# Kernel optimization log

Measured on AMD Instinct MI355X. Metric: run time of the kernel, lower is better.

## Reference

```python
import jax, jax.numpy as jnp
import numpy as np
import math

B, S, E = 2, 2048, 1024
H = 16                      # n_state_heads
STATE_SIZE = 16384
O = math.isqrt(STATE_SIZE // H)   # state_head_order = 32
C = E // (O * H)            # embedding_state_head_order_chunk_size = 2
N_BLOCKS = 12
EPS = 1e-5


def layernorm(x, g):
    mu = jnp.mean(x, axis=-1, keepdims=True)
    var = jnp.mean(jnp.square(x - mu), axis=-1, keepdims=True)
    return (x - mu) * jax.lax.rsqrt(var + EPS) * g


def setup_inputs() -> dict:
    key = jax.random.key(0)
    ks = jax.random.split(key, 8)
    return {
        "activations": jax.random.normal(ks[0], (B, S, E), dtype=jnp.float32),
        # note: torch init zeros W_up; we use small random weights so the scan is non-trivial
        "W_up": jax.random.normal(ks[1], (O, C), dtype=jnp.float32) * 0.02,
        "W_down": jax.random.normal(ks[2], (C, O), dtype=jnp.float32) * (0.02 * math.sqrt(STATE_SIZE)),
        "W_mru": jax.random.normal(ks[3], (E, E), dtype=jnp.float32) * (0.02 / math.sqrt(N_BLOCKS)),
        "g_ln1": jnp.ones((E,), dtype=jnp.float32),
        "g_ln2": jnp.ones((E,), dtype=jnp.float32),
        "W_mlp1": jax.random.normal(ks[4], (4 * E, E), dtype=jnp.float32) * 0.02,
        "W_mlp2": jax.random.normal(ks[5], (E, 4 * E), dtype=jnp.float32) * (0.02 / math.sqrt(N_BLOCKS)),
    }


def reference(activations, W_up, W_down, W_mru, g_ln1, g_ln2, W_mlp1, W_mlp2):
    x = activations                                   # [B,S,E]
    h = layernorm(x, g_ln1)
    hh = h.reshape(B, S, H, O, C)                     # unflatten(-1, (H, O, C))
    # state_matrices_up (Linear C->O, no bias) + eye  -> per-token transition matrices
    M = jnp.einsum('bshoc,qc->bshoq', hh, W_up) + jnp.eye(O, dtype=h.dtype)  # [B,S,H,O,O]
    Mt = jnp.swapaxes(M, 1, 2)                        # [B,H,S,O,O]
    # cumulative non-commutative matrix products along the sequence (log-depth scan)
    P = jax.lax.associative_scan(jnp.matmul, Mt, axis=2)  # P[t] = M_0 @ ... @ M_t
    states = jnp.swapaxes(P, 1, 2)                    # [B,S,H,O,O]
    # state_matrices_down (Linear O->C, no bias), then flatten(-3,-1)
    down = jnp.einsum('bshoq,cq->bshoc', states, W_down).reshape(B, S, E)
    mru_out = down @ W_mru.T
    x = x + mru_out
    y = layernorm(x, g_ln2)
    m = jax.nn.gelu(y @ W_mlp1.T, approximate=False) @ W_mlp2.T
    x = x + m
    new_state = states[-1]                            # faithful to torch states[-1] (last batch element): [S,H,O,O]
    return (x, new_state)
```

## Files before the change

kernel.cpp:

```cpp
#include <hip/hip_runtime.h>
#include <hip/hip_bf16.h>
#include <math.h>

#define Bb 2
#define Ss 2048
#define Ee 1024
#define Hh 16
#define Oo 32
#define Cc 2
#define EPSf 1e-5f
#define NSEG 64
#define SEGL 32
#define NGRP 8
#define GRPL 8

typedef __hip_bfloat16 bf16;
typedef __attribute__((ext_vector_type(8))) short short8;
typedef __attribute__((ext_vector_type(4))) float f32x4;

template <typename OT>
__global__ __launch_bounds__(256) void ln_kernel(const float* __restrict__ x,
                                                 const float* __restrict__ g,
                                                 OT* __restrict__ out) {
    __shared__ float red[8];
    int row = blockIdx.x;
    const float4* xr = (const float4*)(x + (size_t)row * Ee);
    float4 v = xr[threadIdx.x];
    float s = v.x + v.y + v.z + v.w;
#pragma unroll
    for (int off = 32; off > 0; off >>= 1) s += __shfl_xor(s, off);
    int wave = threadIdx.x >> 6, lane = threadIdx.x & 63;
    if (!lane) red[wave] = s;
    __syncthreads();
    float mu = (red[0] + red[1] + red[2] + red[3]) * (1.0f / Ee);
    float dx = v.x - mu, dy = v.y - mu, dz = v.z - mu, dw = v.w - mu;
    float sq = dx * dx + dy * dy + dz * dz + dw * dw;
#pragma unroll
    for (int off = 32; off > 0; off >>= 1) sq += __shfl_xor(sq, off);
    if (!lane) red[wave + 4] = sq;
    __syncthreads();
    float var = (red[4] + red[5] + red[6] + red[7]) * (1.0f / Ee);
    float rs = rsqrtf(var + EPSf);
    float4 gv = ((const float4*)g)[threadIdx.x];
    float o0 = dx * rs * gv.x, o1 = dy * rs * gv.y, o2 = dz * rs * gv.z, o3 = dw * rs * gv.w;
    if constexpr (sizeof(OT) == 4) {
        ((float4*)((float*)out + (size_t)row * Ee))[threadIdx.x] = make_float4(o0, o1, o2, o3);
    } else {
        __align__(8) bf16 t[4] = {__float2bfloat16(o0), __float2bfloat16(o1),
                                  __float2bfloat16(o2), __float2bfloat16(o3)};
        ((ushort4*)((unsigned short*)out + (size_t)row * Ee))[threadIdx.x] = *(const ushort4*)t;
    }
}

__device__ __forceinline__ void cvt4(const float* in, bf16* out, int i) {
    float4 v = ((const float4*)in)[i];
    __align__(8) bf16 t[4] = {__float2bfloat16(v.x), __float2bfloat16(v.y),
                              __float2bfloat16(v.z), __float2bfloat16(v.w)};
    ((ushort4*)out)[i] = *(const ushort4*)t;
}

__global__ __launch_bounds__(256) void prep_kernel(const float* __restrict__ act,
                                                   const float* __restrict__ g,
                                                   float* __restrict__ hs,
                                                   const float* __restrict__ wa, bf16* __restrict__ oa,
                                                   const float* __restrict__ wb, bf16* __restrict__ ob,
                                                   const float* __restrict__ wc, bf16* __restrict__ oc) {
    int bid = blockIdx.x;
    if (bid < Bb * Ss) {
        __shared__ float red[8];
        int row = bid;
        const float4* xr = (const float4*)(act + (size_t)row * Ee);
        float4 v = xr[threadIdx.x];
        float s = v.x + v.y + v.z + v.w;
#pragma unroll
        for (int off = 32; off > 0; off >>= 1) s += __shfl_xor(s, off);
        int wave = threadIdx.x >> 6, lane = threadIdx.x & 63;
        if (!lane) red[wave] = s;
        __syncthreads();
        float mu = (red[0] + red[1] + red[2] + red[3]) * (1.0f / Ee);
        float dx = v.x - mu, dy = v.y - mu, dz = v.z - mu, dw = v.w - mu;
        float sq = dx * dx + dy * dy + dz * dz + dw * dw;
#pragma unroll
        for (int off = 32; off > 0; off >>= 1) sq += __shfl_xor(sq, off);
        if (!lane) red[wave + 4] = sq;
        __syncthreads();
        float var = (red[4] + red[5] + red[6] + red[7]) * (1.0f / Ee);
        float rs = rsqrtf(var + EPSf);
        float4 gv = ((const float4*)g)[threadIdx.x];
        float o0 = dx * rs * gv.x, o1 = dy * rs * gv.y, o2 = dz * rs * gv.z, o3 = dw * rs * gv.w;
        int b = row >> 11, t = row & 2047;
        int e0 = threadIdx.x * 4;
        int head = e0 >> 6;
        float* dst = hs + (((size_t)(b * Hh + head) * Ss) + t) * 64 + (e0 & 63);
        *(float4*)dst = make_float4(o0, o1, o2, o3);
    } else {
        int i = (bid - Bb * Ss) * 256 + threadIdx.x;
        const int nA = (1024 * 1024) / 4;
        const int nB = (4 * 1024 * 1024) / 4;
        if (i < nA) cvt4(wa, oa, i);
        else if (i < nA + nB) cvt4(wb, ob, i - nA);
        else cvt4(wc, oc, i - nA - nB);
    }
}

__device__ __forceinline__ void row_matmul(float e[32], const float* __restrict__ T) {
    float r[32];
#pragma unroll
    for (int q = 0; q < 32; ++q) r[q] = 0.f;
#pragma unroll
    for (int kk = 0; kk < 32; ++kk) {
        float ekk = e[kk];
        const float4* tr = (const float4*)(T + kk * 32);
#pragma unroll
        for (int j = 0; j < 8; ++j) {
            float4 tv = tr[j];
            r[4 * j + 0] = fmaf(ekk, tv.x, r[4 * j + 0]);
            r[4 * j + 1] = fmaf(ekk, tv.y, r[4 * j + 1]);
            r[4 * j + 2] = fmaf(ekk, tv.z, r[4 * j + 2]);
            r[4 * j + 3] = fmaf(ekk, tv.w, r[4 * j + 3]);
        }
    }
#pragma unroll
    for (int q = 0; q < 32; ++q) e[q] = r[q];
}

__global__ __launch_bounds__(256, 2) void scan_pass1(const float* __restrict__ hs,
                                                     const float* __restrict__ Wup,
                                                     float* __restrict__ Ttot) {
    int wv = __builtin_amdgcn_readfirstlane((int)(threadIdx.x >> 6));
    int lane = threadIdx.x & 63;
    int o = lane & 31;
    int seg = blockIdx.x * 4 + wv;
    int chain = seg >> 6;
    int g = seg & 63;

    float wq[64];
#pragma unroll
    for (int j = 0; j < 16; ++j) ((float4*)wq)[j] = ((const float4*)Wup)[j];
    float p[32];
#pragma unroll
    for (int q = 0; q < 32; ++q) p[q] = (q == o) ? 1.0f : 0.0f;

    const float* hb = hs + ((size_t)chain * Ss + (size_t)g * SEGL) * 64;
    float4 ac[16];
#pragma unroll
    for (int j = 0; j < 16; ++j) ac[j] = ((const float4*)hb)[j];

    for (int st = 0; st < SEGL; ++st) {
        float4 an[16];
        if (st + 1 < SEGL) {
            const float4* hn = (const float4*)(hb + (size_t)(st + 1) * 64);
#pragma unroll
            for (int j = 0; j < 16; ++j) an[j] = hn[j];
        }
        float s0 = 0.f, s1 = 0.f, u0 = 0.f, u1 = 0.f;
#pragma unroll
        for (int q = 0; q < 32; q += 2) {
            float4 v = ac[q >> 1];
            s0 = fmaf(p[q], v.x, s0);
            u0 = fmaf(p[q], v.y, u0);
            s1 = fmaf(p[q + 1], v.z, s1);
            u1 = fmaf(p[q + 1], v.w, u1);
        }
        float y0 = s0 + s1, y1 = u0 + u1;
#pragma unroll
        for (int q = 0; q < 32; ++q) p[q] = fmaf(y0, wq[2 * q], fmaf(y1, wq[2 * q + 1], p[q]));
        if (st + 1 < SEGL) {
#pragma unroll
            for (int j = 0; j < 16; ++j) ac[j] = an[j];
        }
    }
    if (lane < 32) {
        float* tb = Ttot + ((size_t)chain * NSEG + g) * 1024 + o * 32;
#pragma unroll
        for (int j = 0; j < 8; ++j)
            ((float4*)tb)[j] = make_float4(p[4 * j], p[4 * j + 1], p[4 * j + 2], p[4 * j + 3]);
    }
}

__global__ __launch_bounds__(512) void scan_pass2(const float* __restrict__ Ttot,
                                                  float* __restrict__ Eexc,
                                                  float* __restrict__ Wkp) {
    __shared__ float Ush[8][1024];
    int chain = blockIdx.x;
    int k = __builtin_amdgcn_readfirstlane((int)(threadIdx.x >> 6));
    int lane = threadIdx.x & 63;
    int o = lane & 31;

    float e[32];
#pragma unroll
    for (int q = 0; q < 32; ++q) e[q] = (q == o) ? 1.0f : 0.0f;
    for (int i = 0; i < GRPL; ++i) {
        int g = k * GRPL + i;
        if (lane < 32) {
            float* eb = Eexc + ((size_t)chain * NSEG + g) * 1024 + o * 32;
#pragma unroll
            for (int j = 0; j < 8; ++j)
                ((float4*)eb)[j] = make_float4(e[4 * j], e[4 * j + 1], e[4 * j + 2], e[4 * j + 3]);
        }
        row_matmul(e, Ttot + ((size_t)chain * NSEG + g) * 1024);
    }
    if (lane < 32) {
        float* ub = &Ush[k][o * 32];
#pragma unroll
        for (int j = 0; j < 8; ++j)
            ((float4*)ub)[j] = make_float4(e[4 * j], e[4 * j + 1], e[4 * j + 2], e[4 * j + 3]);
    }
    __syncthreads();
    float wreg[32];
#pragma unroll
    for (int q = 0; q < 32; ++q) wreg[q] = (q == o) ? 1.0f : 0.0f;
    for (int j = 0; j < k; ++j) row_matmul(wreg, &Ush[j][0]);
    if (lane < 32) {
        float* wb = Wkp + ((size_t)chain * NGRP + k) * 1024 + o * 32;
#pragma unroll
        for (int j = 0; j < 8; ++j)
            ((float4*)wb)[j] = make_float4(wreg[4 * j], wreg[4 * j + 1], wreg[4 * j + 2], wreg[4 * j + 3]);
    }
}

__global__ __launch_bounds__(256, 2) void scan_pass3(const float* __restrict__ hs,
                                                     const float* __restrict__ Wup,
                                                     const float* __restrict__ Wdn,
                                                     const float* __restrict__ Eexc,
                                                     const float* __restrict__ Wkp,
                                                     bf16* __restrict__ down,
                                                     float* __restrict__ state_out) {
    int wv = __builtin_amdgcn_readfirstlane((int)(threadIdx.x >> 6));
    int lane = threadIdx.x & 63;
    int o = lane & 31;
    int seg = blockIdx.x * 4 + wv;
    int chain = seg >> 6;
    int g = seg & 63;
    int b = chain >> 4, head = chain & 15;
    int k = g >> 3;

    float wq[64];
#pragma unroll
    for (int j = 0; j < 16; ++j) ((float4*)wq)[j] = ((const float4*)Wup)[j];
    float wd[64];
#pragma unroll
    for (int j = 0; j < 16; ++j) ((float4*)wd)[j] = ((const float4*)Wdn)[j];

    float G00 = 0.f, G01 = 0.f, G10 = 0.f, G11 = 0.f;
#pragma unroll
    for (int q = 0; q < 32; ++q) {
        G00 = fmaf(wq[2 * q + 0], wd[q], G00);
        G01 = fmaf(wq[2 * q + 0], wd[32 + q], G01);
        G10 = fmaf(wq[2 * q + 1], wd[q], G10);
        G11 = fmaf(wq[2 * q + 1], wd[32 + q], G11);
    }

    float wrow[32];
    const float* wb = Wkp + ((size_t)chain * NGRP + k) * 1024 + o * 32;
#pragma unroll
    for (int j = 0; j < 8; ++j) ((float4*)wrow)[j] = ((const float4*)wb)[j];
    const float* Eb = Eexc + ((size_t)chain * NSEG + g) * 1024;
    float p[32];
#pragma unroll
    for (int q = 0; q < 32; ++q) p[q] = 0.f;
#pragma unroll
    for (int kk = 0; kk < 32; ++kk) {
        float wkk = wrow[kk];
        const float4* er = (const float4*)(Eb + kk * 32);
#pragma unroll
        for (int j = 0; j < 8; ++j) {
            float4 ev = er[j];
            p[4 * j + 0] = fmaf(wkk, ev.x, p[4 * j + 0]);
            p[4 * j + 1] = fmaf(wkk, ev.y, p[4 * j + 1]);
            p[4 * j + 2] = fmaf(wkk, ev.z, p[4 * j + 2]);
            p[4 * j + 3] = fmaf(wkk, ev.w, p[4 * j + 3]);
        }
    }

    float d0 = 0.f, d1 = 0.f;
#pragma unroll
    for (int q = 0; q < 32; ++q) {
        d0 = fmaf(p[q], wd[q], d0);
        d1 = fmaf(p[q], wd[32 + q], d1);
    }

    const float* hb = hs + ((size_t)chain * Ss + (size_t)g * SEGL) * 64;
    bf16* db = down + ((size_t)b * Ss + (size_t)g * SEGL) * Ee + head * 64 + o * 2;
    float* sb = state_out + ((size_t)g * SEGL * Hh + head) * 1024 + o * 32;

    float4 ac[16];
#pragma unroll
    for (int j = 0; j < 16; ++j) ac[j] = ((const float4*)hb)[j];

    for (int st = 0; st < SEGL; ++st) {
        float4 an[16];
        if (st + 1 < SEGL) {
            const float4* hn = (const float4*)(hb + (size_t)(st + 1) * 64);
#pragma unroll
            for (int j = 0; j < 16; ++j) an[j] = hn[j];
        }
        float s0 = 0.f, s1 = 0.f, u0 = 0.f, u1 = 0.f;
#pragma unroll
        for (int q = 0; q < 32; q += 2) {
            float4 v = ac[q >> 1];
            s0 = fmaf(p[q], v.x, s0);
            u0 = fmaf(p[q], v.y, u0);
            s1 = fmaf(p[q + 1], v.z, s1);
            u1 = fmaf(p[q + 1], v.w, u1);
        }
        float y0 = s0 + s1, y1 = u0 + u1;
#pragma unroll
        for (int q = 0; q < 32; ++q) p[q] = fmaf(y0, wq[2 * q], fmaf(y1, wq[2 * q + 1], p[q]));
        d0 = fmaf(y0, G00, fmaf(y1, G10, d0));
        d1 = fmaf(y0, G01, fmaf(y1, G11, d1));
        if (lane < 32) {
            __hip_bfloat162 dv;
            dv.x = __float2bfloat16(d0);
            dv.y = __float2bfloat16(d1);
            *(__hip_bfloat162*)(db + (size_t)st * Ee) = dv;
            if (b == Bb - 1) {
                float* sp = sb + (size_t)st * (Hh * 1024);
#pragma unroll
                for (int j = 0; j < 8; ++j)
                    ((float4*)sp)[j] = make_float4(p[4 * j], p[4 * j + 1], p[4 * j + 2], p[4 * j + 3]);
            }
        }
        if (st + 1 < SEGL) {
#pragma unroll
            for (int j = 0; j < 16; ++j) ac[j] = an[j];
        }
    }
}

__device__ __forceinline__ void load_lds16(const bf16* g, short* l) {
    __builtin_amdgcn_global_load_lds((const __attribute__((address_space(1))) unsigned int*)g,
                                     (__attribute__((address_space(3))) unsigned int*)l,
                                     16, 0, 0);
}

template <bool GELU, bool RESID, bool BF16OUT>
__global__ __launch_bounds__(256, 2) void mgemm64(const bf16* __restrict__ A,
                                                  const bf16* __restrict__ Wt,
                                                  const float* __restrict__ res,
                                                  float* __restrict__ Cf,
                                                  bf16* __restrict__ Cb,
                                                  int M, int N, int K) {
    __shared__ __align__(16) short As[3][64 * 32];
    __shared__ __align__(16) short Bs[3][128 * 32];
    int tid = threadIdx.x;
    int w = __builtin_amdgcn_readfirstlane(tid >> 6);
    int l = tid & 63;

    int nbm = M >> 6, nbn = N >> 7;
    int nwg = nbm * nbn;
    int cpx = nwg >> 3;
    int v = ((int)blockIdx.x & 7) * cpx + ((int)blockIdx.x >> 3);
    int sq = v >> 6, rem = v & 63;
    int sqPerRow = nbn >> 3;
    int bm = (sq / sqPerRow) * 8 + (rem >> 3);
    int bn = (sq % sqPerRow) * 8 + (rem & 7);

    int wr = w >> 1, wc = w & 1;
    int lr = l & 15;
    int lks = (((l >> 4) ^ ((lr >> 1) & 3)) * 8);

    int srow = tid >> 2;
    int scol = ((tid & 3) ^ ((tid >> 3) & 3)) * 8;
    const bf16* ga  = A + (size_t)(bm * 64 + srow) * K + scol;
    const bf16* gb0 = Wt + (size_t)(bn * 128 + srow) * K + scol;
    const bf16* gb1 = Wt + (size_t)(bn * 128 + 64 + srow) * K + scol;

    f32x4 acc[2][4];
#pragma unroll
    for (int m = 0; m < 2; ++m)
#pragma unroll
        for (int n = 0; n < 4; ++n) acc[m][n] = (f32x4){0.f, 0.f, 0.f, 0.f};

#define STAGE64(d, kt)                                       \
    do {                                                     \
        int _off = (kt) * 32;                                \
        load_lds16(ga + _off, &As[d][w * 512]);              \
        load_lds16(gb0 + _off, &Bs[d][w * 512]);             \
        load_lds16(gb1 + _off, &Bs[d][2048 + w * 512]);      \
    } while (0)

    const int NK = K >> 5;
    STAGE64(0, 0);
    STAGE64(1, 1);
    STAGE64(2, 2);
    asm volatile("s_waitcnt vmcnt(6)" ::: "memory");
    __builtin_amdgcn_sched_barrier(0);
    __builtin_amdgcn_s_barrier();

    for (int t = 0; t < NK; ++t) {
        int d = t % 3;
        short8 af[2], bfr[4];
#pragma unroll
        for (int m = 0; m < 2; ++m)
            af[m] = *(const short8*)&As[d][(wr * 32 + m * 16 + lr) * 32 + lks];
#pragma unroll
        for (int n = 0; n < 4; ++n)
            bfr[n] = *(const short8*)&Bs[d][(wc * 64 + n * 16 + lr) * 32 + lks];
        asm volatile("s_waitcnt lgkmcnt(0)" ::: "memory");
        __builtin_amdgcn_sched_barrier(0);
        __builtin_amdgcn_s_barrier();
        if (t + 3 < NK) STAGE64(d, t + 3);
        __builtin_amdgcn_sched_barrier(0);
        __builtin_amdgcn_s_setprio(1);
#pragma unroll
        for (int m = 0; m < 2; ++m)
#pragma unroll
            for (int n = 0; n < 4; ++n)
                acc[m][n] = __builtin_amdgcn_mfma_f32_16x16x32_bf16(af[m], bfr[n], acc[m][n], 0, 0, 0);
        __builtin_amdgcn_s_setprio(0);
        if (t + 3 < NK) {
            asm volatile("s_waitcnt vmcnt(6)" ::: "memory");
        } else if (t + 2 < NK) {
            asm volatile("s_waitcnt vmcnt(3)" ::: "memory");
        } else if (t + 1 < NK) {
            asm volatile("s_waitcnt vmcnt(0)" ::: "memory");
        }
        __builtin_amdgcn_sched_barrier(0);
        __builtin_amdgcn_s_barrier();
    }
#undef STAGE64

#pragma unroll
    for (int m = 0; m < 2; ++m) {
#pragma unroll
        for (int n = 0; n < 4; ++n) {
            int gr0 = bm * 64 + wr * 32 + m * 16 + (l >> 4) * 4;
            int gc = bn * 128 + wc * 64 + n * 16 + lr;
#pragma unroll
            for (int j = 0; j < 4; ++j) {
                float v2 = acc[m][n][j];
                if (GELU) v2 = 0.5f * v2 * (1.0f + erff(v2 * 0.70710678118654752f));
                if (RESID) v2 += res[(size_t)(gr0 + j) * N + gc];
                if (BF16OUT) Cb[(size_t)(gr0 + j) * N + gc] = __float2bfloat16(v2);
                else Cf[(size_t)(gr0 + j) * N + gc] = v2;
            }
        }
    }
}

__global__ __launch_bounds__(512, 1) void mgemm8(const bf16* __restrict__ A,
                                                 const bf16* __restrict__ Wt,
                                                 bf16* __restrict__ Cb,
                                                 int M, int N, int K) {
    __shared__ __align__(16) short As[4][256 * 32];
    __shared__ __align__(16) short Bs[4][256 * 32];
    int tid = threadIdx.x;
    int w = __builtin_amdgcn_readfirstlane(tid >> 6);
    int l = tid & 63;

    int nbm = M >> 8, nbn = N >> 8;
    int nwg = nbm * nbn;
    int cpx = nwg >> 3;
    int v = ((int)blockIdx.x & 7) * cpx + ((int)blockIdx.x >> 3);
    int sq = v >> 6, rem = v & 63;
    int sqPerRow = nbn >> 3;
    int bm = (sq / sqPerRow) * 8 + (rem >> 3);
    int bn = (sq % sqPerRow) * 8 + (rem & 7);

    int wr = w >> 2, wc = w & 3;
    int lr = l & 15;
    int lks = (((l >> 4) ^ ((lr >> 1) & 3)) * 8);

    int srow = tid >> 2;
    int scol = ((tid & 3) ^ ((tid >> 3) & 3)) * 8;
    const bf16* ga0 = A + (size_t)(bm * 256 + srow) * K + scol;
    const bf16* ga1 = A + (size_t)(bm * 256 + 128 + srow) * K + scol;
    const bf16* gb0 = Wt + (size_t)(bn * 256 + srow) * K + scol;
    const bf16* gb1 = Wt + (size_t)(bn * 256 + 128 + srow) * K + scol;

    f32x4 acc[8][4];
#pragma unroll
    for (int m = 0; m < 8; ++m)
#pragma unroll
        for (int n = 0; n < 4; ++n) acc[m][n] = (f32x4){0.f, 0.f, 0.f, 0.f};

#define STAGE_A(d, kt)                                       \
    do {                                                     \
        int _off = (kt) * 32;                                \
        load_lds16(ga0 + _off, &As[d][w * 512]);             \
        load_lds16(ga1 + _off, &As[d][4096 + w * 512]);      \
    } while (0)
#define STAGE_B(d, kt)                                       \
    do {                                                     \
        int _off = (kt) * 32;                                \
        load_lds16(gb0 + _off, &Bs[d][w * 512]);             \
        load_lds16(gb1 + _off, &Bs[d][4096 + w * 512]);      \
    } while (0)

    const int NK = K >> 5;
    STAGE_A(0, 0); STAGE_B(0, 0);
    STAGE_A(1, 1); STAGE_B(1, 1);
    STAGE_A(2, 2); STAGE_B(2, 2);
    asm volatile("s_waitcnt vmcnt(8)" ::: "memory");
    __builtin_amdgcn_sched_barrier(0);
    __builtin_amdgcn_s_barrier();

    for (int t = 0; t < NK; ++t) {
        int d = t & 3;
        short8 af[8], bfr[4];
#pragma unroll
        for (int n = 0; n < 4; ++n)
            bfr[n] = *(const short8*)&Bs[d][(wc * 64 + n * 16 + lr) * 32 + lks];
#pragma unroll
        for (int m = 0; m < 4; ++m)
            af[m] = *(const short8*)&As[d][(wr * 128 + m * 16 + lr) * 32 + lks];
        if (t + 3 < NK) STAGE_A((t + 3) & 3, t + 3);
        __builtin_amdgcn_sched_barrier(0);
        __builtin_amdgcn_s_barrier();
        asm volatile("s_waitcnt lgkmcnt(0)" ::: "memory");
        __builtin_amdgcn_sched_barrier(0);
        __builtin_amdgcn_s_setprio(1);
#pragma unroll
        for (int m = 0; m < 4; ++m)
#pragma unroll
            for (int n = 0; n < 4; ++n)
                acc[m][n] = __builtin_amdgcn_mfma_f32_16x16x32_bf16(af[m], bfr[n], acc[m][n], 0, 0, 0);
        __builtin_amdgcn_s_setprio(0);
        __builtin_amdgcn_s_barrier();
#pragma unroll
        for (int m = 4; m < 8; ++m)
            af[m] = *(const short8*)&As[d][(wr * 128 + m * 16 + lr) * 32 + lks];
        if (t + 3 < NK) STAGE_B((t + 3) & 3, t + 3);
        __builtin_amdgcn_sched_barrier(0);
        __builtin_amdgcn_s_barrier();
        asm volatile("s_waitcnt lgkmcnt(0)" ::: "memory");
        __builtin_amdgcn_sched_barrier(0);
        __builtin_amdgcn_s_setprio(1);
#pragma unroll
        for (int m = 4; m < 8; ++m)
#pragma unroll
            for (int n = 0; n < 4; ++n)
                acc[m][n] = __builtin_amdgcn_mfma_f32_16x16x32_bf16(af[m], bfr[n], acc[m][n], 0, 0, 0);
        __builtin_amdgcn_s_setprio(0);
        if (t + 3 < NK) {
            asm volatile("s_waitcnt vmcnt(8)" ::: "memory");
        } else if (t + 2 < NK) {
            asm volatile("s_waitcnt vmcnt(4)" ::: "memory");
        } else if (t + 1 < NK) {
            asm volatile("s_waitcnt vmcnt(0)" ::: "memory");
        }
        __builtin_amdgcn_sched_barrier(0);
        __builtin_amdgcn_s_barrier();
    }
#undef STAGE_A
#undef STAGE_B

#pragma unroll
    for (int m = 0; m < 8; ++m) {
#pragma unroll
        for (int n = 0; n < 4; ++n) {
            int gr0 = bm * 256 + wr * 128 + m * 16 + (l >> 4) * 4;
            int gc = bn * 256 + wc * 64 + n * 16 + lr;
#pragma unroll
            for (int j = 0; j < 4; ++j) {
                float vv = acc[m][n][j];
                vv = 0.5f * vv * (1.0f + erff(vv * 0.70710678118654752f));
                Cb[(size_t)(gr0 + j) * N + gc] = __float2bfloat16(vv);
            }
        }
    }
}

extern "C" void kernel_launch(void* const* d_in, const int* in_sizes, int n_in,
                              void* d_out, int out_size, void* d_ws, size_t ws_size,
                              hipStream_t stream) {
    const float* act    = (const float*)d_in[0];
    const float* W_up   = (const float*)d_in[1];
    const float* W_down = (const float*)d_in[2];
    const float* W_mru  = (const float*)d_in[3];
    const float* g_ln1  = (const float*)d_in[4];
    const float* g_ln2  = (const float*)d_in[5];
    const float* W_mlp1 = (const float*)d_in[6];
    const float* W_mlp2 = (const float*)d_in[7];

    float* out_x     = (float*)d_out;
    float* out_state = (float*)d_out + (size_t)Bb * Ss * Ee;

    float* wsf = (float*)d_ws;
    const size_t Mfl = 1024 * 1024;
    float* hs       = wsf;
    bf16*  down_bf  = (bf16*)(wsf + 4 * Mfl);
    bf16*  y_bf     = (bf16*)(wsf + 6 * Mfl);
    bf16*  t1_bf    = (bf16*)(wsf + 8 * Mfl);
    float* Ttot = wsf + 8 * Mfl;
    float* Eexc = wsf + 10 * Mfl;
    float* Wkp  = wsf + 12 * Mfl;
    bf16*  Wmru_bf  = (bf16*)(wsf + 16 * Mfl);
    bf16*  Wmlp1_bf = (bf16*)(wsf + 17 * Mfl);
    bf16*  Wmlp2_bf = (bf16*)(wsf + 19 * Mfl);

    const int MT = Bb * Ss;

    prep_kernel<<<MT + 9216, 256, 0, stream>>>(act, g_ln1, hs,
                                               W_mru, Wmru_bf, W_mlp1, Wmlp1_bf, W_mlp2, Wmlp2_bf);
    scan_pass1<<<512, 256, 0, stream>>>(hs, W_up, Ttot);
    scan_pass2<<<32, 512, 0, stream>>>(Ttot, Eexc, Wkp);
    scan_pass3<<<512, 256, 0, stream>>>(hs, W_up, W_down, Eexc, Wkp, down_bf, out_state);
    mgemm64<false, true, false><<<(MT / 64) * (Ee / 128), 256, 0, stream>>>(
        down_bf, Wmru_bf, act, out_x, nullptr, MT, Ee, Ee);
    ln_kernel<bf16><<<MT, 256, 0, stream>>>(out_x, g_ln2, y_bf);
    mgemm8<<<(MT / 256) * (4 * Ee / 256), 512, 0, stream>>>(
        y_bf, Wmlp1_bf, t1_bf, MT, 4 * Ee, Ee);
    mgemm64<false, true, false><<<(MT / 64) * (Ee / 128), 256, 0, stream>>>(
        t1_bf, Wmlp2_bf, out_x, out_x, nullptr, MT, Ee, 4 * Ee);
}
```

Before: 338.6 us.

## Fuse three scan passes into one kernel with one block per chain

Merges scan_pass1, scan_pass2 and scan_pass3 into a single scan_fused kernel. It launches one 512-thread block per chain (32 blocks), and each wave processes 8 segments one after another; block-level barriers replace the kernel boundaries between phases. This removes two kernel launches and the global-memory handoff latency between them. In exchange, the grid shrinks from 512 blocks to 32, which cuts parallelism and lengthens each wave's serial chain about eightfold.

```diff
diff --git a/kernel.cpp b/kernel.cpp
--- a/kernel.cpp
+++ b/kernel.cpp
@@ -124,124 +124,106 @@
     for (int q = 0; q < 32; ++q) e[q] = r[q];
 }
 
-__global__ __launch_bounds__(256, 2) void scan_pass1(const float* __restrict__ hs,
+__global__ __launch_bounds__(512, 2) void scan_fused(const float* __restrict__ hs,
                                                      const float* __restrict__ Wup,
-                                                     float* __restrict__ Ttot) {
-    int wv = __builtin_amdgcn_readfirstlane((int)(threadIdx.x >> 6));
-    int lane = threadIdx.x & 63;
-    int o = lane & 31;
-    int seg = blockIdx.x * 4 + wv;
-    int chain = seg >> 6;
-    int g = seg & 63;
-
-    float wq[64];
-#pragma unroll
-    for (int j = 0; j < 16; ++j) ((float4*)wq)[j] = ((const float4*)Wup)[j];
-    float p[32];
-#pragma unroll
-    for (int q = 0; q < 32; ++q) p[q] = (q == o) ? 1.0f : 0.0f;
-
-    const float* hb = hs + ((size_t)chain * Ss + (size_t)g * SEGL) * 64;
-    float4 ac[16];
-#pragma unroll
-    for (int j = 0; j < 16; ++j) ac[j] = ((const float4*)hb)[j];
-
-    for (int st = 0; st < SEGL; ++st) {
-        float4 an[16];
-        if (st + 1 < SEGL) {
-            const float4* hn = (const float4*)(hb + (size_t)(st + 1) * 64);
-#pragma unroll
-            for (int j = 0; j < 16; ++j) an[j] = hn[j];
-        }
-        float s0 = 0.f, s1 = 0.f, u0 = 0.f, u1 = 0.f;
-#pragma unroll
-        for (int q = 0; q < 32; q += 2) {
-            float4 v = ac[q >> 1];
-            s0 = fmaf(p[q], v.x, s0);
-            u0 = fmaf(p[q], v.y, u0);
-            s1 = fmaf(p[q + 1], v.z, s1);
-            u1 = fmaf(p[q + 1], v.w, u1);
-        }
-        float y0 = s0 + s1, y1 = u0 + u1;
-#pragma unroll
-        for (int q = 0; q < 32; ++q) p[q] = fmaf(y0, wq[2 * q], fmaf(y1, wq[2 * q + 1], p[q]));
-        if (st + 1 < SEGL) {
-#pragma unroll
-            for (int j = 0; j < 16; ++j) ac[j] = an[j];
-        }
-    }
-    if (lane < 32) {
-        float* tb = Ttot + ((size_t)chain * NSEG + g) * 1024 + o * 32;
-#pragma unroll
-        for (int j = 0; j < 8; ++j)
-            ((float4*)tb)[j] = make_float4(p[4 * j], p[4 * j + 1], p[4 * j + 2], p[4 * j + 3]);
-    }
-}
-
-__global__ __launch_bounds__(512) void scan_pass2(const float* __restrict__ Ttot,
-                                                  float* __restrict__ Eexc,
-                                                  float* __restrict__ Wkp) {
+                                                     const float* __restrict__ Wdn,
+                                                     float* __restrict__ Ttot,
+                                                     float* __restrict__ Eexc,
+                                                     float* __restrict__ Wkp,
+                                                     bf16* __restrict__ down,
+                                                     float* __restrict__ state_out) {
     __shared__ float Ush[8][1024];
     int chain = blockIdx.x;
-    int k = __builtin_amdgcn_readfirstlane((int)(threadIdx.x >> 6));
-    int lane = threadIdx.x & 63;
+    int tid = threadIdx.x;
+    int wv = __builtin_amdgcn_readfirstlane(tid >> 6);
+    int lane = tid & 63;
     int o = lane & 31;
-
-    float e[32];
-#pragma unroll
-    for (int q = 0; q < 32; ++q) e[q] = (q == o) ? 1.0f : 0.0f;
-    for (int i = 0; i < GRPL; ++i) {
-        int g = k * GRPL + i;
+    int b = chain >> 4, head = chain & 15;
+
+    float wq[64];
+#pragma unroll
+    for (int j = 0; j < 16; ++j) ((float4*)wq)[j] = ((const float4*)Wup)[j];
+
+    for (int i = 0; i < 8; ++i) {
+        int g = wv * 8 + i;
+        float p[32];
+#pragma unroll
+        for (int q = 0; q < 32; ++q) p[q] = (q == o) ? 1.0f : 0.0f;
+        const float* hb = hs + ((size_t)chain * Ss + (size_t)g * SEGL) * 64;
+        float4 ac[16];
+#pragma unroll
+        for (int j = 0; j < 16; ++j) ac[j] = ((const float4*)hb)[j];
+        for (int st = 0; st < SEGL; ++st) {
+            float4 an[16];
+            if (st + 1 < SEGL) {
+                const float4* hn = (const float4*)(hb + (size_t)(st + 1) * 64);
+#pragma unroll
+                for (int j = 0; j < 16; ++j) an[j] = hn[j];
+            }
+            float s0 = 0.f, s1 = 0.f, u0 = 0.f, u1 = 0.f;
+#pragma unroll
+            for (int q = 0; q < 32; q += 2) {
+                float4 v = ac[q >> 1];
+                s0 = fmaf(p[q], v.x, s0);
+                u0 = fmaf(p[q], v.y, u0);
+                s1 = fmaf(p[q + 1], v.z, s1);
+                u1 = fmaf(p[q + 1], v.w, u1);
+            }
+            float y0 = s0 + s1, y1 = u0 + u1;
+#pragma unroll
+            for (int q = 0; q < 32; ++q) p[q] = fmaf(y0, wq[2 * q], fmaf(y1, wq[2 * q + 1], p[q]));
+            if (st + 1 < SEGL) {
+#pragma unroll
+                for (int j = 0; j < 16; ++j) ac[j] = an[j];
+            }
+        }
         if (lane < 32) {
-            float* eb = Eexc + ((size_t)chain * NSEG + g) * 1024 + o * 32;
+            float* tb = Ttot + ((size_t)chain * NSEG + g) * 1024 + o * 32;
 #pragma unroll
             for (int j = 0; j < 8; ++j)
-                ((float4*)eb)[j] = make_float4(e[4 * j], e[4 * j + 1], e[4 * j + 2], e[4 * j + 3]);
-        }
-        row_matmul(e, Ttot + ((size_t)chain * NSEG + g) * 1024);
-    }
-    if (lane < 32) {
-        float* ub = &Ush[k][o * 32];
-#pragma unroll
-        for (int j = 0; j < 8; ++j)
-            ((float4*)ub)[j] = make_float4(e[4 * j], e[4 * j + 1], e[4 * j + 2], e[4 * j + 3]);
+                ((float4*)tb)[j] = make_float4(p[4 * j], p[4 * j + 1], p[4 * j + 2], p[4 * j + 3]);
+        }
     }
     __syncthreads();
-    float wreg[32];
-#pragma unroll
-    for (int q = 0; q < 32; ++q) wreg[q] = (q == o) ? 1.0f : 0.0f;
-    for (int j = 0; j < k; ++j) row_matmul(wreg, &Ush[j][0]);
-    if (lane < 32) {
-        float* wb = Wkp + ((size_t)chain * NGRP + k) * 1024 + o * 32;
-#pragma unroll
-        for (int j = 0; j < 8; ++j)
-            ((float4*)wb)[j] = make_float4(wreg[4 * j], wreg[4 * j + 1], wreg[4 * j + 2], wreg[4 * j + 3]);
-    }
-}
-
-__global__ __launch_bounds__(256, 2) void scan_pass3(const float* __restrict__ hs,
-                                                     const float* __restrict__ Wup,
-                                                     const float* __restrict__ Wdn,
-                                                     const float* __restrict__ Eexc,
-                                                     const float* __restrict__ Wkp,
-                                                     bf16* __restrict__ down,
-                                                     float* __restrict__ state_out) {
-    int wv = __builtin_amdgcn_readfirstlane((int)(threadIdx.x >> 6));
-    int lane = threadIdx.x & 63;
-    int o = lane & 31;
-    int seg = blockIdx.x * 4 + wv;
-    int chain = seg >> 6;
-    int g = seg & 63;
-    int b = chain >> 4, head = chain & 15;
-    int k = g >> 3;
-
-    float wq[64];
-#pragma unroll
-    for (int j = 0; j < 16; ++j) ((float4*)wq)[j] = ((const float4*)Wup)[j];
+
+    {
+        int k = wv;
+        float e[32];
+#pragma unroll
+        for (int q = 0; q < 32; ++q) e[q] = (q == o) ? 1.0f : 0.0f;
+        for (int i = 0; i < GRPL; ++i) {
+            int g = k * GRPL + i;
+            if (lane < 32) {
+                float* eb = Eexc + ((size_t)chain * NSEG + g) * 1024 + o * 32;
+#pragma unroll
+                for (int j = 0; j < 8; ++j)
+                    ((float4*)eb)[j] = make_float4(e[4 * j], e[4 * j + 1], e[4 * j + 2], e[4 * j + 3]);
+            }
+            row_matmul(e, Ttot + ((size_t)chain * NSEG + g) * 1024);
+        }
+        if (lane < 32) {
+            float* ub = &Ush[k][o * 32];
+#pragma unroll
+            for (int j = 0; j < 8; ++j)
+                ((float4*)ub)[j] = make_float4(e[4 * j], e[4 * j + 1], e[4 * j + 2], e[4 * j + 3]);
+        }
+        __syncthreads();
+        float wreg[32];
+#pragma unroll
+        for (int q = 0; q < 32; ++q) wreg[q] = (q == o) ? 1.0f : 0.0f;
+        for (int j = 0; j < k; ++j) row_matmul(wreg, &Ush[j][0]);
+        if (lane < 32) {
+            float* wb = Wkp + ((size_t)chain * NGRP + k) * 1024 + o * 32;
+#pragma unroll
+            for (int j = 0; j < 8; ++j)
+                ((float4*)wb)[j] = make_float4(wreg[4 * j], wreg[4 * j + 1], wreg[4 * j + 2], wreg[4 * j + 3]);
+        }
+    }
+    __syncthreads();
+
     float wd[64];
 #pragma unroll
     for (int j = 0; j < 16; ++j) ((float4*)wd)[j] = ((const float4*)Wdn)[j];
-
     float G00 = 0.f, G01 = 0.f, G10 = 0.f, G11 = 0.f;
 #pragma unroll
     for (int q = 0; q < 32; ++q) {
@@ -251,79 +233,84 @@
         G11 = fmaf(wq[2 * q + 1], wd[32 + q], G11);
     }
 
-    float wrow[32];
-    const float* wb = Wkp + ((size_t)chain * NGRP + k) * 1024 + o * 32;
-#pragma unroll
-    for (int j = 0; j < 8; ++j) ((float4*)wrow)[j] = ((const float4*)wb)[j];
-    const float* Eb = Eexc + ((size_t)chain * NSEG + g) * 1024;
-    float p[32];
-#pragma unroll
-    for (int q = 0; q < 32; ++q) p[q] = 0.f;
-#pragma unroll
-    for (int kk = 0; kk < 32; ++kk) {
-        float wkk = wrow[kk];
-        const float4* er = (const float4*)(Eb + kk * 32);
-#pragma unroll
-        for (int j = 0; j < 8; ++j) {
-            float4 ev = er[j];
-            p[4 * j + 0] = fmaf(wkk, ev.x, p[4 * j + 0]);
-            p[4 * j + 1] = fmaf(wkk, ev.y, p[4 * j + 1]);
-            p[4 * j + 2] = fmaf(wkk, ev.z, p[4 * j + 2]);
-            p[4 * j + 3] = fmaf(wkk, ev.w, p[4 * j + 3]);
-        }
-    }
-
-    float d0 = 0.f, d1 = 0.f;
-#pragma unroll
-    for (int q = 0; q < 32; ++q) {
-        d0 = fmaf(p[q], wd[q], d0);
-        d1 = fmaf(p[q], wd[32 + q], d1);
-    }
-
-    const float* hb = hs + ((size_t)chain * Ss + (size_t)g * SEGL) * 64;
-    bf16* db = down + ((size_t)b * Ss + (size_t)g * SEGL) * Ee + head * 64 + o * 2;
-    float* sb = state_out + ((size_t)g * SEGL * Hh + head) * 1024 + o * 32;
-
-    float4 ac[16];
-#pragma unroll
-    for (int j = 0; j < 16; ++j) ac[j] = ((const float4*)hb)[j];
-
-    for (int st = 0; st < SEGL; ++st) {
-        float4 an[16];
-        if (st + 1 < SEGL) {
-            const float4* hn = (const float4*)(hb + (size_t)(st + 1) * 64);
-#pragma unroll
-            for (int j = 0; j < 16; ++j) an[j] = hn[j];
-        }
-        float s0 = 0.f, s1 = 0.f, u0 = 0.f, u1 = 0.f;
-#pragma unroll
-        for (int q = 0; q < 32; q += 2) {
-            float4 v = ac[q >> 1];
-            s0 = fmaf(p[q], v.x, s0);
-            u0 = fmaf(p[q], v.y, u0);
-            s1 = fmaf(p[q + 1], v.z, s1);
-            u1 = fmaf(p[q + 1], v.w, u1);
-        }
-        float y0 = s0 + s1, y1 = u0 + u1;
-#pragma unroll
-        for (int q = 0; q < 32; ++q) p[q] = fmaf(y0, wq[2 * q], fmaf(y1, wq[2 * q + 1], p[q]));
-        d0 = fmaf(y0, G00, fmaf(y1, G10, d0));
-        d1 = fmaf(y0, G01, fmaf(y1, G11, d1));
-        if (lane < 32) {
-            __hip_bfloat162 dv;
-            dv.x = __float2bfloat16(d0);
-            dv.y = __float2bfloat16(d1);
-            *(__hip_bfloat162*)(db + (size_t)st * Ee) = dv;
-            if (b == Bb - 1) {
-                float* sp = sb + (size_t)st * (Hh * 1024);
-#pragma unroll
-                for (int j = 0; j < 8; ++j)
-                    ((float4*)sp)[j] = make_float4(p[4 * j], p[4 * j + 1], p[4 * j + 2], p[4 * j + 3]);
-            }
-        }
-        if (st + 1 < SEGL) {
-#pragma unroll
-            for (int j = 0; j < 16; ++j) ac[j] = an[j];
+    for (int i = 0; i < 8; ++i) {
+        int g = wv * 8 + i;
+        int k = g >> 3;
+
+        float wrow[32];
+        const float* wb = Wkp + ((size_t)chain * NGRP + k) * 1024 + o * 32;
+#pragma unroll
+        for (int j = 0; j < 8; ++j) ((float4*)wrow)[j] = ((const float4*)wb)[j];
+        const float* Eb = Eexc + ((size_t)chain * NSEG + g) * 1024;
+        float p[32];
+#pragma unroll
+        for (int q = 0; q < 32; ++q) p[q] = 0.f;
+#pragma unroll
+        for (int kk = 0; kk < 32; ++kk) {
+            float wkk = wrow[kk];
+            const float4* er = (const float4*)(Eb + kk * 32);
+#pragma unroll
+            for (int j = 0; j < 8; ++j) {
+                float4 ev = er[j];
+                p[4 * j + 0] = fmaf(wkk, ev.x, p[4 * j + 0]);
+                p[4 * j + 1] = fmaf(wkk, ev.y, p[4 * j + 1]);
+                p[4 * j + 2] = fmaf(wkk, ev.z, p[4 * j + 2]);
+                p[4 * j + 3] = fmaf(wkk, ev.w, p[4 * j + 3]);
+            }
+        }
+
+        float d0 = 0.f, d1 = 0.f;
+#pragma unroll
+        for (int q = 0; q < 32; ++q) {
+            d0 = fmaf(p[q], wd[q], d0);
+            d1 = fmaf(p[q], wd[32 + q], d1);
+        }
+
+        const float* hb = hs + ((size_t)chain * Ss + (size_t)g * SEGL) * 64;
+        bf16* db = down + ((size_t)b * Ss + (size_t)g * SEGL) * Ee + head * 64 + o * 2;
+        float* sb = state_out + ((size_t)g * SEGL * Hh + head) * 1024 + o * 32;
+
+        float4 ac[16];
+#pragma unroll
+        for (int j = 0; j < 16; ++j) ac[j] = ((const float4*)hb)[j];
+
+        for (int st = 0; st < SEGL; ++st) {
+            float4 an[16];
+            if (st + 1 < SEGL) {
+                const float4* hn = (const float4*)(hb + (size_t)(st + 1) * 64);
+#pragma unroll
+                for (int j = 0; j < 16; ++j) an[j] = hn[j];
+            }
+            float s0 = 0.f, s1 = 0.f, u0 = 0.f, u1 = 0.f;
+#pragma unroll
+            for (int q = 0; q < 32; q += 2) {
+                float4 v = ac[q >> 1];
+                s0 = fmaf(p[q], v.x, s0);
+                u0 = fmaf(p[q], v.y, u0);
+                s1 = fmaf(p[q + 1], v.z, s1);
+                u1 = fmaf(p[q + 1], v.w, u1);
+            }
+            float y0 = s0 + s1, y1 = u0 + u1;
+#pragma unroll
+            for (int q = 0; q < 32; ++q) p[q] = fmaf(y0, wq[2 * q], fmaf(y1, wq[2 * q + 1], p[q]));
+            d0 = fmaf(y0, G00, fmaf(y1, G10, d0));
+            d1 = fmaf(y0, G01, fmaf(y1, G11, d1));
+            if (lane < 32) {
+                __hip_bfloat162 dv;
+                dv.x = __float2bfloat16(d0);
+                dv.y = __float2bfloat16(d1);
+                *(__hip_bfloat162*)(db + (size_t)st * Ee) = dv;
+                if (b == Bb - 1) {
+                    float* sp = sb + (size_t)st * (Hh * 1024);
+#pragma unroll
+                    for (int j = 0; j < 8; ++j)
+                        ((float4*)sp)[j] = make_float4(p[4 * j], p[4 * j + 1], p[4 * j + 2], p[4 * j + 3]);
+                }
+            }
+            if (st + 1 < SEGL) {
+#pragma unroll
+                for (int j = 0; j < 16; ++j) ac[j] = an[j];
+            }
         }
     }
 }
@@ -594,9 +581,7 @@
 
     prep_kernel<<<MT + 9216, 256, 0, stream>>>(act, g_ln1, hs,
                                                W_mru, Wmru_bf, W_mlp1, Wmlp1_bf, W_mlp2, Wmlp2_bf);
-    scan_pass1<<<512, 256, 0, stream>>>(hs, W_up, Ttot);
-    scan_pass2<<<32, 512, 0, stream>>>(Ttot, Eexc, Wkp);
-    scan_pass3<<<512, 256, 0, stream>>>(hs, W_up, W_down, Eexc, Wkp, down_bf, out_state);
+    scan_fused<<<32, 512, 0, stream>>>(hs, W_up, W_down, Ttot, Eexc, Wkp, down_bf, out_state);
     mgemm64<false, true, false><<<(MT / 64) * (Ee / 128), 256, 0, stream>>>(
         down_bf, Wmru_bf, act, out_x, nullptr, MT, Ee, Ee);
     ln_kernel<bf16><<<MT, 256, 0, stream>>>(out_x, g_ln2, y_bf);
```

New measurement: 1.169 ms. 245% more time.
